# Optimization experiments

Hardware: AMD Instinct MI355X
Metric: run time of the kernel (lower is better)

Reference implementation:

```python
import jax, jax.numpy as jnp
import numpy as np

N, S, E, H = 2, 2048, 1024, 16
D = E // H  # head_dim = 64


def setup_inputs() -> dict:
    key = jax.random.key(0)
    k1, k2, k3 = jax.random.split(key, 3)
    x = jax.random.normal(k1, (N, S, E), dtype=jnp.float32)
    # Xavier-uniform-scaled weights (torch Linear layout: [out_features, in_features])
    lim_qkv = (6.0 / (E + 3 * E)) ** 0.5
    qkv_w = jax.random.uniform(k2, (3 * E, E), dtype=jnp.float32, minval=-lim_qkv, maxval=lim_qkv)
    lim_o = (6.0 / (E + E)) ** 0.5
    o_w = jax.random.uniform(k3, (E, E), dtype=jnp.float32, minval=-lim_o, maxval=lim_o)
    # causal look-ahead mask: positions where mask == 0 are excluded
    attn_mask = jnp.tril(jnp.ones((S, S), dtype=jnp.int32))
    return {"x": x, "attn_mask": attn_mask, "qkv_w": qkv_w, "o_w": o_w}


def reference(x, attn_mask, qkv_w, o_w):
    n, s, e = x.shape
    qkv = x @ qkv_w.T                              # (N, S, 3E)
    q, k, v = jnp.split(qkv, 3, axis=-1)
    # (N, S, E) -> (N, H, S, D)
    def to_heads(t):
        return t.reshape(n, s, H, D).transpose(0, 2, 1, 3)
    q, k, v = to_heads(q), to_heads(k), to_heads(v)
    scale = 1.0 / jnp.sqrt(jnp.asarray(D, dtype=x.dtype))
    logits = jnp.einsum('bhqd,bhkd->bhqk', q, k) * scale   # (N, H, S, S)
    mask = attn_mask.reshape(1, 1, s, s)                    # expand_mask: 2D -> (1,1,S,S)
    logits = jnp.where(mask == 0, -jnp.inf, logits)
    attn_weights = jax.nn.softmax(logits, axis=-1)
    values = jnp.einsum('bhqk,bhkd->bhqd', attn_weights, v)  # (N, H, S, D)
    values = values.transpose(0, 2, 1, 3).reshape(n, s, e)
    o = values @ o_w.T
    return o
```

## Files before the change

### kernel.cpp

```cpp
#include <hip/hip_runtime.h>
#include <math.h>

typedef unsigned short u16;
typedef unsigned int uint;
typedef __attribute__((ext_vector_type(8))) short bf16x8;
typedef __attribute__((ext_vector_type(8))) _Float16 half8;
typedef __attribute__((ext_vector_type(2))) _Float16 half2t;
typedef __attribute__((ext_vector_type(4))) float floatx4;

__device__ __forceinline__ u16 f2bf(float f) {
  union { float f; uint u; } c; c.f = f;
  return (u16)((c.u + 0x7FFFu + ((c.u >> 16) & 1u)) >> 16);
}
__device__ __forceinline__ float bf2f(u16 h) {
  union { uint u; float f; } c; c.u = ((uint)h) << 16;
  return c.f;
}
__device__ __forceinline__ u16 h2u(_Float16 h) {
  union { _Float16 h; u16 u; } c; c.h = h;
  return c.u;
}

#if __has_builtin(__builtin_amdgcn_exp2f)
#define EX2 __builtin_amdgcn_exp2f
#else
#define EX2 exp2f
#endif

__device__ __forceinline__ void gl_lds16(const u16* g, u16* l) {
  __builtin_amdgcn_global_load_lds(
      (const __attribute__((address_space(1))) uint*)g,
      (__attribute__((address_space(3))) uint*)l, 16, 0, 0);
}

__device__ __forceinline__ void store_c(u16* p, float v) { *p = f2bf(v); }
__device__ __forceinline__ void store_c(float* p, float v) { *p = v; }

#define ROR16(x, n)                                                        \
  __builtin_bit_cast(float, __builtin_amdgcn_update_dpp(                   \
      __builtin_bit_cast(int, (x)), __builtin_bit_cast(int, (x)),          \
      0x120 + (n), 0xF, 0xF, false))
__device__ __forceinline__ float rsum16(float x) {
  x += ROR16(x, 8); x += ROR16(x, 4); x += ROR16(x, 2); x += ROR16(x, 1);
  return x;
}

__global__ __launch_bounds__(256) void cvt_all(const float* __restrict__ x,
                                               const float* __restrict__ qw,
                                               const float* __restrict__ ow,
                                               u16* __restrict__ xb,
                                               u16* __restrict__ wb,
                                               u16* __restrict__ ob) {
  int bx = blockIdx.x;
  const float* src; u16* dst; int off;
  if (bx < 2048) { src = x; dst = xb; off = bx; }
  else if (bx < 3584) { src = qw; dst = wb; off = bx - 2048; }
  else { src = ow; dst = ob; off = bx - 3584; }
  int i = (off * 256 + threadIdx.x) * 8;
  float4 a = *(const float4*)(src + i);
  float4 b = *(const float4*)(src + i + 4);
  bf16x8 r;
  r[0] = (short)f2bf(a.x); r[1] = (short)f2bf(a.y);
  r[2] = (short)f2bf(a.z); r[3] = (short)f2bf(a.w);
  r[4] = (short)f2bf(b.x); r[5] = (short)f2bf(b.y);
  r[6] = (short)f2bf(b.z); r[7] = (short)f2bf(b.w);
  *(bf16x8*)(dst + i) = r;
}

__global__ __launch_bounds__(256) void vtrans(const u16* __restrict__ qkv,
                                              u16* __restrict__ vt) {
  constexpr int S = 2048, E = 1024, TE = 3072;
  __shared__ u16 tile[64 * 72];
  const int t = threadIdx.x;
  const int kv0 = blockIdx.x * 64;
  const int bh = blockIdx.y, b = bh >> 4, h = bh & 15;
  const u16* src = qkv + (size_t)b * S * TE + 2 * E + h * 64;
#pragma unroll
  for (int i = 0; i < 2; ++i) {
    int c = t + i * 256;
    int kv = c >> 3, d0 = (c & 7) * 8;
    *(bf16x8*)&tile[kv * 72 + d0] = *(const bf16x8*)&src[(size_t)(kv0 + kv) * TE + d0];
  }
  __syncthreads();
  u16* dst = vt + (size_t)bh * 64 * S + kv0;
#pragma unroll
  for (int i = 0; i < 2; ++i) {
    int c = t + i * 256;
    int d = c >> 3, k0 = (c & 7) * 8;
    bf16x8 r;
#pragma unroll
    for (int j = 0; j < 8; ++j)
      r[j] = (short)h2u((_Float16)bf2f(tile[(k0 + j) * 72 + d]));
    *(bf16x8*)&dst[(size_t)d * S + k0] = r;
  }
}

template <typename TC>
__global__ __launch_bounds__(256) void gemm_bt(const u16* __restrict__ A,
                                               const u16* __restrict__ B,
                                               TC* __restrict__ C,
                                               int K, int N) {
  __shared__ __align__(16) u16 lds_a[128 * 64];
  __shared__ __align__(16) u16 lds_b[128 * 64];
  const int t = threadIdx.x;
  const int w = t >> 6, lane = t & 63, quad = lane >> 4, lr = lane & 15;
  const int wr = w >> 1, wc = w & 1;
  const int m0 = blockIdx.y * 128, n0 = blockIdx.x * 128;

  const int srow = lane >> 3;
  const int scol = ((lane & 7) ^ srow) * 8;
  const u16* Ab = A + (size_t)(m0 + w * 32 + srow) * K + scol;
  const u16* Bb = B + (size_t)(n0 + w * 32 + srow) * K + scol;
  u16* la = lds_a + (w * 32) * 64;
  u16* lb = lds_b + (w * 32) * 64;

  floatx4 acc[4][4];
#pragma unroll
  for (int i = 0; i < 4; ++i)
#pragma unroll
    for (int j = 0; j < 4; ++j) acc[i][j] = {0.f, 0.f, 0.f, 0.f};

  for (int k0 = 0; k0 < K; k0 += 64) {
#pragma unroll
    for (int j = 0; j < 4; ++j) {
      gl_lds16(Ab + (size_t)(j * 8) * K + k0, la + j * 8 * 64);
      gl_lds16(Bb + (size_t)(j * 8) * K + k0, lb + j * 8 * 64);
    }
    __syncthreads();
#pragma unroll
    for (int kk = 0; kk < 2; ++kk) {
      bf16x8 af[4], bfr[4];
#pragma unroll
      for (int mi = 0; mi < 4; ++mi)
        af[mi] = *(const bf16x8*)&lds_a[(wr * 64 + mi * 16 + lr) * 64 +
                                        (((kk * 4 + quad) ^ (lr & 7)) * 8)];
#pragma unroll
      for (int ni = 0; ni < 4; ++ni)
        bfr[ni] = *(const bf16x8*)&lds_b[(wc * 64 + ni * 16 + lr) * 64 +
                                         (((kk * 4 + quad) ^ (lr & 7)) * 8)];
#pragma unroll
      for (int mi = 0; mi < 4; ++mi)
#pragma unroll
        for (int ni = 0; ni < 4; ++ni)
          acc[mi][ni] = __builtin_amdgcn_mfma_f32_16x16x32_bf16(
              af[mi], bfr[ni], acc[mi][ni], 0, 0, 0);
    }
    __syncthreads();
  }
#pragma unroll
  for (int mi = 0; mi < 4; ++mi)
#pragma unroll
    for (int r = 0; r < 4; ++r) {
      int m = m0 + wr * 64 + mi * 16 + quad * 4 + r;
#pragma unroll
      for (int ni = 0; ni < 4; ++ni) {
        int n = n0 + wc * 64 + ni * 16 + lr;
        store_c(&C[(size_t)m * N + n], acc[mi][ni][r]);
      }
    }
}

template <typename TC>
__global__ __launch_bounds__(256) void gemm_bt64(const u16* __restrict__ A,
                                                 const u16* __restrict__ B,
                                                 TC* __restrict__ C,
                                                 int K, int N) {
  __shared__ __align__(16) u16 lds_a[64 * 64];
  __shared__ __align__(16) u16 lds_b[128 * 64];
  const int t = threadIdx.x;
  const int w = t >> 6, lane = t & 63, quad = lane >> 4, lr = lane & 15;
  const int m0 = blockIdx.y * 64, n0 = blockIdx.x * 128;

  const int srow = lane >> 3;
  const int scol = ((lane & 7) ^ srow) * 8;
  const u16* Ab = A + (size_t)(m0 + srow) * K + scol;
  const u16* Bb = B + (size_t)(n0 + srow) * K + scol;

  floatx4 acc[4][2];
#pragma unroll
  for (int i = 0; i < 4; ++i)
#pragma unroll
    for (int j = 0; j < 2; ++j) acc[i][j] = {0.f, 0.f, 0.f, 0.f};

  for (int k0 = 0; k0 < K; k0 += 64) {
#pragma unroll
    for (int i = 0; i < 2; ++i)
      gl_lds16(Ab + (size_t)((w * 2 + i) * 8) * K + k0, &lds_a[(w * 2 + i) * 8 * 64]);
#pragma unroll
    for (int i = 0; i < 4; ++i)
      gl_lds16(Bb + (size_t)((w * 4 + i) * 8) * K + k0, &lds_b[(w * 4 + i) * 8 * 64]);
    __syncthreads();
#pragma unroll
    for (int kk = 0; kk < 2; ++kk) {
      bf16x8 af[4], bfr[2];
#pragma unroll
      for (int mi = 0; mi < 4; ++mi)
        af[mi] = *(const bf16x8*)&lds_a[(mi * 16 + lr) * 64 +
                                        (((kk * 4 + quad) ^ (lr & 7)) * 8)];
#pragma unroll
      for (int ni = 0; ni < 2; ++ni)
        bfr[ni] = *(const bf16x8*)&lds_b[(w * 32 + ni * 16 + lr) * 64 +
                                         (((kk * 4 + quad) ^ (lr & 7)) * 8)];
#pragma unroll
      for (int mi = 0; mi < 4; ++mi)
#pragma unroll
        for (int ni = 0; ni < 2; ++ni)
          acc[mi][ni] = __builtin_amdgcn_mfma_f32_16x16x32_bf16(
              af[mi], bfr[ni], acc[mi][ni], 0, 0, 0);
    }
    __syncthreads();
  }
#pragma unroll
  for (int mi = 0; mi < 4; ++mi)
#pragma unroll
    for (int r = 0; r < 4; ++r) {
      int m = m0 + mi * 16 + quad * 4 + r;
#pragma unroll
      for (int ni = 0; ni < 2; ++ni) {
        int n = n0 + w * 32 + ni * 16 + lr;
        store_c(&C[(size_t)m * N + n], acc[mi][ni][r]);
      }
    }
}

__global__ __launch_bounds__(256, 2) void attn_fwd(const u16* __restrict__ qkv,
                                                   const u16* __restrict__ vt,
                                                   u16* __restrict__ out,
                                                   float* __restrict__ opart,
                                                   float* __restrict__ lpart) {
  constexpr int S = 2048, E = 1024, TE = 3072;
  constexpr float NEG = -1e30f;
  __shared__ __align__(16) u16 lds_k[2][128 * 64];
  __shared__ __align__(16) u16 lds_vt[2][64 * 128];
  const int t = threadIdx.x;
  const int w = t >> 6, lane = t & 63, quad = lane >> 4, lr = lane & 15;
  const int bx = (int)blockIdx.x;
  const int h = bx & 15, pr = (bx >> 4) & 7, hB = (bx >> 7) & 1, b = bx >> 8;
  const int qtH = 15 - pr;
  const int bh = b * 16 + h;
  const int pid = bh * 8 + pr;
  const size_t base = (size_t)b * S * TE;
  const u16* kbase = qkv + base + E + h * 64;
  const u16* vtb = vt + (size_t)bh * 64 * S;

  const int s8 = lane >> 3;
  const int kcol = ((lane & 7) ^ s8) * 8;
  const int vrow = lane >> 4;

  const int n0 = hB ? (8 - pr) : 8;
  const int niter = hB ? 9 : 8;

  const float QS = 0.125f * 1.44269504f;
  bf16x8 qf[2][2];
  float lst2[2];
  floatx4 oacc[2][4];

  auto load_q = [&](int qt) {
#pragma unroll
    for (int rg = 0; rg < 2; ++rg)
#pragma unroll
      for (int kk = 0; kk < 2; ++kk) {
        bf16x8 q = *(const bf16x8*)&qkv[base +
            (size_t)(qt * 128 + w * 32 + rg * 16 + lr) * TE + h * 64 + kk * 32 + quad * 8];
#pragma unroll
        for (int jj = 0; jj < 8; ++jj) q[jj] = (short)f2bf(bf2f((u16)q[jj]) * QS);
        qf[rg][kk] = q;
      }
  };
  auto reset_acc = [&]() {
    lst2[0] = 0.f; lst2[1] = 0.f;
#pragma unroll
    for (int rg = 0; rg < 2; ++rg)
#pragma unroll
      for (int di = 0; di < 4; ++di) oacc[rg][di] = {0.f, 0.f, 0.f, 0.f};
  };
  auto reduce_l = [&](float* lred) {
#pragma unroll
    for (int rg = 0; rg < 2; ++rg) {
      float x = lst2[rg];
      x += __shfl_xor(x, 16);
      x += __shfl_xor(x, 32);
      lred[rg] = x;
    }
  };
  auto emit_partial = [&](int slot) {
    float lred[2];
    reduce_l(lred);
    float* op = opart + ((size_t)slot * 256 + pid) * (128 * 64);
    float* lp = lpart + ((size_t)slot * 256 + pid) * 128;
    if (quad == 0) lp[w * 32 + lr] = lred[0];
    if (quad == 1) lp[w * 32 + 16 + lr] = lred[1];
#pragma unroll
    for (int rg = 0; rg < 2; ++rg)
#pragma unroll
      for (int r = 0; r < 4; ++r) {
        int row = w * 32 + rg * 16 + quad * 4 + r;
#pragma unroll
        for (int di = 0; di < 4; ++di)
          op[row * 64 + di * 16 + lr] = oacc[rg][di][r];
      }
  };
  auto kv_of = [&](int it) -> int {
    if (!hB) return it;
    return (it < n0) ? (8 + it) : (it - n0);
  };
  auto stage = [&](int kvt, int bi) {
    int nb = kvt * 128;
#pragma unroll
    for (int i = 0; i < 4; ++i) {
      int p0 = w * 8 + i * 32;
      int p = p0 + s8;
      int kv = ((p >> 5) & 3) * 32 + ((p >> 2) & 3) * 8 + ((p >> 4) & 1) * 4 + (p & 3);
      gl_lds16(kbase + (size_t)(nb + kv) * TE + kcol, &lds_k[bi][p0 * 64]);
    }
#pragma unroll
    for (int i = 0; i < 4; ++i) {
      int d0 = w * 4 + i * 16;
      int d = d0 + vrow;
      int cbg = ((lane & 15) ^ (d & 15)) * 8;
      gl_lds16(vtb + (size_t)d * S + nb + cbg, &lds_vt[bi][d0 * 128]);
    }
  };

  load_q(qtH);
  stage(kv_of(0), 0);
  reset_acc();

  for (int it = 0; it < niter; ++it) {
    const int cur = it & 1;
    const int kt = kv_of(it);
    const int qcur = (hB && it >= n0) ? pr : qtH;

    asm volatile("s_waitcnt vmcnt(0)\n\ts_barrier" ::: "memory");
    __builtin_amdgcn_sched_barrier(0);

    floatx4 st[2][8];
#pragma unroll
    for (int rg = 0; rg < 2; ++rg)
#pragma unroll
      for (int ni = 0; ni < 8; ++ni) st[rg][ni] = {-4.f, -4.f, -4.f, -4.f};
    __builtin_amdgcn_s_setprio(1);
#pragma unroll
    for (int kk = 0; kk < 2; ++kk) {
      bf16x8 kb[8];
#pragma unroll
      for (int ni = 0; ni < 8; ++ni)
        kb[ni] = *(const bf16x8*)&lds_k[cur][(ni * 16 + lr) * 64 +
                                            (((kk * 4 + quad) ^ (lr & 7)) * 8)];
#pragma unroll
      for (int rg = 0; rg < 2; ++rg)
#pragma unroll
        for (int ni = 0; ni < 8; ++ni)
          st[rg][ni] = __builtin_amdgcn_mfma_f32_16x16x32_bf16(
              kb[ni], qf[rg][kk], st[rg][ni], 0, 0, 0);
    }
    __builtin_amdgcn_s_setprio(0);

    half8 vb[4][4];
#pragma unroll
    for (int kk = 0; kk < 4; ++kk)
#pragma unroll
      for (int di = 0; di < 4; ++di)
        vb[kk][di] = *(const half8*)&lds_vt[cur][(di * 16 + lr) * 128 +
                                                 (((kk * 4 + quad) ^ lr) << 3)];

    if (it + 1 < niter) stage(kv_of(it + 1), cur ^ 1);

    const bool diag = (kt == qcur);
#pragma unroll
    for (int rg = 0; rg < 2; ++rg) {
      const int rloc = w * 32 + rg * 16 + lr;
      float ex[8][4];
#pragma unroll
      for (int ni = 0; ni < 8; ++ni)
#pragma unroll
        for (int rr = 0; rr < 4; ++rr) {
          float s = st[rg][ni][rr];
          if (diag) {
            int kvl = ((ni >> 1) << 5) + (quad << 3) + ((ni & 1) << 2) + rr;
            if (kvl > rloc) s = NEG;
          }
          ex[ni][rr] = EX2(s);
        }
      float tsum[8];
#pragma unroll
      for (int ni = 0; ni < 8; ++ni)
        tsum[ni] = (ex[ni][0] + ex[ni][1]) + (ex[ni][2] + ex[ni][3]);
      lst2[rg] += ((tsum[0] + tsum[1]) + (tsum[2] + tsum[3])) +
                  ((tsum[4] + tsum[5]) + (tsum[6] + tsum[7]));
      __builtin_amdgcn_s_setprio(1);
#pragma unroll
      for (int c = 0; c < 4; ++c) {
        union { half2t h2[4]; half8 h8; } pu;
        pu.h2[0] = __builtin_bit_cast(half2t,
            __builtin_amdgcn_cvt_pkrtz(ex[2 * c][0], ex[2 * c][1]));
        pu.h2[1] = __builtin_bit_cast(half2t,
            __builtin_amdgcn_cvt_pkrtz(ex[2 * c][2], ex[2 * c][3]));
        pu.h2[2] = __builtin_bit_cast(half2t,
            __builtin_amdgcn_cvt_pkrtz(ex[2 * c + 1][0], ex[2 * c + 1][1]));
        pu.h2[3] = __builtin_bit_cast(half2t,
            __builtin_amdgcn_cvt_pkrtz(ex[2 * c + 1][2], ex[2 * c + 1][3]));
#pragma unroll
        for (int di = 0; di < 4; ++di)
          oacc[rg][di] = __builtin_amdgcn_mfma_f32_16x16x32_f16(
              pu.h8, vb[c][di], oacc[rg][di], 0, 0, 0);
      }
      __builtin_amdgcn_s_setprio(0);
    }

    if (hB && it == n0 - 1) {
      emit_partial(1);
      reset_acc();
      load_q(pr);
    }
  }

  if (!hB) {
    emit_partial(0);
  } else {
    float lred[2];
    reduce_l(lred);
#pragma unroll
    for (int rg = 0; rg < 2; ++rg)
#pragma unroll
      for (int r = 0; r < 4; ++r) {
        int sg = pr * 128 + w * 32 + rg * 16 + quad * 4 + r;
        float lrow = __shfl(lred[rg], quad * 4 + r);
        float inv_l = 1.f / lrow;
#pragma unroll
        for (int di = 0; di < 4; ++di)
          out[((size_t)(b * S + sg)) * E + h * 64 + di * 16 + lr] =
              f2bf(oacc[rg][di][r] * inv_l);
      }
  }
}

__global__ __launch_bounds__(256) void attn_combine(const float* __restrict__ opart,
                                                    const float* __restrict__ lpart,
                                                    u16* __restrict__ out) {
  constexpr int S = 2048, E = 1024;
  const int p = (int)blockIdx.x;
  const int pr = p & 7, bh = p >> 3, h = bh & 15, b = bh >> 4;
  const int q0 = (15 - pr) * 128;
  const int t = threadIdx.x;
  const int row = t >> 1, c0 = (t & 1) * 32;
  const float* o0 = opart + (size_t)p * (128 * 64) + row * 64 + c0;
  const float* o1 = o0 + (size_t)256 * 128 * 64;
  float l = lpart[p * 128 + row] + lpart[256 * 128 + p * 128 + row];
  float inv = 1.f / l;
  u16* dst = out + ((size_t)(b * S + q0 + row)) * E + h * 64 + c0;
#pragma unroll
  for (int i = 0; i < 4; ++i) {
    float4 a0 = ((const float4*)o0)[2 * i], a1 = ((const float4*)o0)[2 * i + 1];
    float4 b0 = ((const float4*)o1)[2 * i], b1 = ((const float4*)o1)[2 * i + 1];
    bf16x8 r;
    r[0] = (short)f2bf((a0.x + b0.x) * inv);
    r[1] = (short)f2bf((a0.y + b0.y) * inv);
    r[2] = (short)f2bf((a0.z + b0.z) * inv);
    r[3] = (short)f2bf((a0.w + b0.w) * inv);
    r[4] = (short)f2bf((a1.x + b1.x) * inv);
    r[5] = (short)f2bf((a1.y + b1.y) * inv);
    r[6] = (short)f2bf((a1.z + b1.z) * inv);
    r[7] = (short)f2bf((a1.w + b1.w) * inv);
    ((bf16x8*)dst)[i] = r;
  }
}

extern "C" void kernel_launch(void* const* d_in, const int* in_sizes, int n_in,
                              void* d_out, int out_size, void* d_ws, size_t ws_size,
                              hipStream_t stream) {
  constexpr int NB = 2, S = 2048, E = 1024;
  constexpr int M = NB * S;
  const float* x = (const float*)d_in[0];
  const float* qkv_w = (const float*)d_in[2];
  const float* o_w = (const float*)d_in[3];
  float* out = (float*)d_out;

  u16* qkv = (u16*)d_ws;
  u16* vt = qkv + (size_t)M * 3 * E;
  u16* xb = vt + (size_t)32 * 64 * S;
  u16* attn_o = xb;
  u16* wb = xb + (size_t)M * E;
  u16* ob = wb + (size_t)3 * E * E;
  float* opart = (float*)(ob + (size_t)E * E);
  float* lpart = opart + (size_t)2 * 256 * 128 * 64;

  cvt_all<<<4096, 256, 0, stream>>>(x, qkv_w, o_w, xb, wb, ob);
  gemm_bt<u16><<<dim3(3 * E / 128, M / 128), 256, 0, stream>>>(xb, wb, qkv, E, 3 * E);
  vtrans<<<dim3(S / 64, NB * 16), 256, 0, stream>>>(qkv, vt);
  attn_fwd<<<512, 256, 0, stream>>>(qkv, vt, attn_o, opart, lpart);
  attn_combine<<<256, 256, 0, stream>>>(opart, lpart, attn_o);
  gemm_bt64<float><<<dim3(E / 128, M / 64), 256, 0, stream>>>(attn_o, ob, out, E, E);
}
```

Measured before the change: 198.6 us.

## Split causal attention into four KV chunks per pair with atomic accumulation

The attention work for each pair of query tiles (17 KV tiles) is now split across four blocks instead of two, giving 1024 blocks. Each block adds its unnormalized output and row sums into a zeroed global fp32 buffer with atomicAdd, and a normalize kernel writes the bf16 result. LDS is single-buffered with an extra barrier, and launch bounds ask for four blocks per CU, which trades load/compute overlap for occupancy. The change adds a memset, atomic traffic and non-deterministic summation order.

New measurement: 502.8 us. 2.53x slower.

```diff
diff --git a/kernel.cpp b/kernel.cpp
--- a/kernel.cpp
+++ b/kernel.cpp
@@ -35,15 +35,6 @@
 
 __device__ __forceinline__ void store_c(u16* p, float v) { *p = f2bf(v); }
 __device__ __forceinline__ void store_c(float* p, float v) { *p = v; }
-
-#define ROR16(x, n)                                                        \
-  __builtin_bit_cast(float, __builtin_amdgcn_update_dpp(                   \
-      __builtin_bit_cast(int, (x)), __builtin_bit_cast(int, (x)),          \
-      0x120 + (n), 0xF, 0xF, false))
-__device__ __forceinline__ float rsum16(float x) {
-  x += ROR16(x, 8); x += ROR16(x, 4); x += ROR16(x, 2); x += ROR16(x, 1);
-  return x;
-}
 
 __global__ __launch_bounds__(256) void cvt_all(const float* __restrict__ x,
                                                const float* __restrict__ qw,
@@ -223,22 +214,20 @@
     }
 }
 
-__global__ __launch_bounds__(256, 2) void attn_fwd(const u16* __restrict__ qkv,
+__global__ __launch_bounds__(256, 4) void attn_fwd(const u16* __restrict__ qkv,
                                                    const u16* __restrict__ vt,
-                                                   u16* __restrict__ out,
-                                                   float* __restrict__ opart,
-                                                   float* __restrict__ lpart) {
+                                                   float* __restrict__ oaccg,
+                                                   float* __restrict__ laccg) {
   constexpr int S = 2048, E = 1024, TE = 3072;
   constexpr float NEG = -1e30f;
-  __shared__ __align__(16) u16 lds_k[2][128 * 64];
-  __shared__ __align__(16) u16 lds_vt[2][64 * 128];
+  __shared__ __align__(16) u16 lds_k[128 * 64];
+  __shared__ __align__(16) u16 lds_vt[64 * 128];
   const int t = threadIdx.x;
   const int w = t >> 6, lane = t & 63, quad = lane >> 4, lr = lane & 15;
   const int bx = (int)blockIdx.x;
-  const int h = bx & 15, pr = (bx >> 4) & 7, hB = (bx >> 7) & 1, b = bx >> 8;
+  const int h = bx & 15, qr = (bx >> 4) & 3, pr = (bx >> 6) & 7, b = bx >> 9;
   const int qtH = 15 - pr;
   const int bh = b * 16 + h;
-  const int pid = bh * 8 + pr;
   const size_t base = (size_t)b * S * TE;
   const u16* kbase = qkv + base + E + h * 64;
   const u16* vtb = vt + (size_t)bh * 64 * S;
@@ -247,8 +236,9 @@
   const int kcol = ((lane & 7) ^ s8) * 8;
   const int vrow = lane >> 4;
 
-  const int n0 = hB ? (8 - pr) : 8;
-  const int niter = hB ? 9 : 8;
+  const int fs = qr * 4;
+  const int fe = (qr == 3) ? 17 : fs + 4;
+  const int bnd = 16 - pr;
 
   const float QS = 0.125f * 1.44269504f;
   bf16x8 qf[2][2];
@@ -283,13 +273,13 @@
       lred[rg] = x;
     }
   };
-  auto emit_partial = [&](int slot) {
+  auto emit_atomic = [&](int qt) {
     float lred[2];
     reduce_l(lred);
-    float* op = opart + ((size_t)slot * 256 + pid) * (128 * 64);
-    float* lp = lpart + ((size_t)slot * 256 + pid) * 128;
-    if (quad == 0) lp[w * 32 + lr] = lred[0];
-    if (quad == 1) lp[w * 32 + 16 + lr] = lred[1];
+    float* oa = oaccg + ((size_t)(bh * 16 + qt)) * (128 * 64);
+    float* la = laccg + (bh * 16 + qt) * 128;
+    if (quad == 0) atomicAdd(&la[w * 32 + lr], lred[0]);
+    if (quad == 1) atomicAdd(&la[w * 32 + 16 + lr], lred[1]);
 #pragma unroll
     for (int rg = 0; rg < 2; ++rg)
 #pragma unroll
@@ -297,40 +287,33 @@
         int row = w * 32 + rg * 16 + quad * 4 + r;
 #pragma unroll
         for (int di = 0; di < 4; ++di)
-          op[row * 64 + di * 16 + lr] = oacc[rg][di][r];
+          atomicAdd(&oa[row * 64 + di * 16 + lr], oacc[rg][di][r]);
       }
   };
-  auto kv_of = [&](int it) -> int {
-    if (!hB) return it;
-    return (it < n0) ? (8 + it) : (it - n0);
-  };
-  auto stage = [&](int kvt, int bi) {
+  auto stage = [&](int kvt) {
     int nb = kvt * 128;
 #pragma unroll
     for (int i = 0; i < 4; ++i) {
       int p0 = w * 8 + i * 32;
       int p = p0 + s8;
       int kv = ((p >> 5) & 3) * 32 + ((p >> 2) & 3) * 8 + ((p >> 4) & 1) * 4 + (p & 3);
-      gl_lds16(kbase + (size_t)(nb + kv) * TE + kcol, &lds_k[bi][p0 * 64]);
+      gl_lds16(kbase + (size_t)(nb + kv) * TE + kcol, &lds_k[p0 * 64]);
     }
 #pragma unroll
     for (int i = 0; i < 4; ++i) {
       int d0 = w * 4 + i * 16;
       int d = d0 + vrow;
       int cbg = ((lane & 15) ^ (d & 15)) * 8;
-      gl_lds16(vtb + (size_t)d * S + nb + cbg, &lds_vt[bi][d0 * 128]);
+      gl_lds16(vtb + (size_t)d * S + nb + cbg, &lds_vt[d0 * 128]);
     }
   };
 
-  load_q(qtH);
-  stage(kv_of(0), 0);
+  int qcur = (fs < bnd) ? qtH : pr;
+  load_q(qcur);
   reset_acc();
-
-  for (int it = 0; it < niter; ++it) {
-    const int cur = it & 1;
-    const int kt = kv_of(it);
-    const int qcur = (hB && it >= n0) ? pr : qtH;
-
+  stage((fs < bnd) ? fs : fs - bnd);
+
+  for (int f = fs; f < fe; ++f) {
     asm volatile("s_waitcnt vmcnt(0)\n\ts_barrier" ::: "memory");
     __builtin_amdgcn_sched_barrier(0);
 
@@ -345,8 +328,8 @@
       bf16x8 kb[8];
 #pragma unroll
       for (int ni = 0; ni < 8; ++ni)
-        kb[ni] = *(const bf16x8*)&lds_k[cur][(ni * 16 + lr) * 64 +
-                                            (((kk * 4 + quad) ^ (lr & 7)) * 8)];
+        kb[ni] = *(const bf16x8*)&lds_k[(ni * 16 + lr) * 64 +
+                                        (((kk * 4 + quad) ^ (lr & 7)) * 8)];
 #pragma unroll
       for (int rg = 0; rg < 2; ++rg)
 #pragma unroll
@@ -361,12 +344,18 @@
     for (int kk = 0; kk < 4; ++kk)
 #pragma unroll
       for (int di = 0; di < 4; ++di)
-        vb[kk][di] = *(const half8*)&lds_vt[cur][(di * 16 + lr) * 128 +
-                                                 (((kk * 4 + quad) ^ lr) << 3)];
-
-    if (it + 1 < niter) stage(kv_of(it + 1), cur ^ 1);
-
-    const bool diag = (kt == qcur);
+        vb[kk][di] = *(const half8*)&lds_vt[(di * 16 + lr) * 128 +
+                                            (((kk * 4 + quad) ^ lr) << 3)];
+
+    asm volatile("s_waitcnt lgkmcnt(0)\n\ts_barrier" ::: "memory");
+    __builtin_amdgcn_sched_barrier(0);
+
+    if (f + 1 < fe) {
+      int f2 = f + 1;
+      stage((f2 < bnd) ? f2 : f2 - bnd);
+    }
+
+    const bool diag = (f == bnd - 1) || (f == 16);
 #pragma unroll
     for (int rg = 0; rg < 2; ++rg) {
       const int rloc = w * 32 + rg * 16 + lr;
@@ -408,60 +397,40 @@
       __builtin_amdgcn_s_setprio(0);
     }
 
-    if (hB && it == n0 - 1) {
-      emit_partial(1);
+    if (f == bnd - 1 && f + 1 < fe) {
+      emit_atomic(qtH);
       reset_acc();
       load_q(pr);
-    }
-  }
-
-  if (!hB) {
-    emit_partial(0);
-  } else {
-    float lred[2];
-    reduce_l(lred);
-#pragma unroll
-    for (int rg = 0; rg < 2; ++rg)
-#pragma unroll
-      for (int r = 0; r < 4; ++r) {
-        int sg = pr * 128 + w * 32 + rg * 16 + quad * 4 + r;
-        float lrow = __shfl(lred[rg], quad * 4 + r);
-        float inv_l = 1.f / lrow;
-#pragma unroll
-        for (int di = 0; di < 4; ++di)
-          out[((size_t)(b * S + sg)) * E + h * 64 + di * 16 + lr] =
-              f2bf(oacc[rg][di][r] * inv_l);
-      }
-  }
-}
-
-__global__ __launch_bounds__(256) void attn_combine(const float* __restrict__ opart,
-                                                    const float* __restrict__ lpart,
-                                                    u16* __restrict__ out) {
+      qcur = pr;
+    }
+  }
+
+  emit_atomic(qcur);
+}
+
+__global__ __launch_bounds__(256) void attn_norm(const float* __restrict__ oaccg,
+                                                 const float* __restrict__ laccg,
+                                                 u16* __restrict__ out) {
   constexpr int S = 2048, E = 1024;
   const int p = (int)blockIdx.x;
-  const int pr = p & 7, bh = p >> 3, h = bh & 15, b = bh >> 4;
-  const int q0 = (15 - pr) * 128;
+  const int qt = p & 15, bh = p >> 4, h = bh & 15, b = bh >> 4;
   const int t = threadIdx.x;
   const int row = t >> 1, c0 = (t & 1) * 32;
-  const float* o0 = opart + (size_t)p * (128 * 64) + row * 64 + c0;
-  const float* o1 = o0 + (size_t)256 * 128 * 64;
-  float l = lpart[p * 128 + row] + lpart[256 * 128 + p * 128 + row];
-  float inv = 1.f / l;
-  u16* dst = out + ((size_t)(b * S + q0 + row)) * E + h * 64 + c0;
+  const float* o = oaccg + (size_t)p * (128 * 64) + row * 64 + c0;
+  float inv = 1.f / laccg[p * 128 + row];
+  u16* dst = out + ((size_t)(b * S + qt * 128 + row)) * E + h * 64 + c0;
 #pragma unroll
   for (int i = 0; i < 4; ++i) {
-    float4 a0 = ((const float4*)o0)[2 * i], a1 = ((const float4*)o0)[2 * i + 1];
-    float4 b0 = ((const float4*)o1)[2 * i], b1 = ((const float4*)o1)[2 * i + 1];
+    float4 a0 = ((const float4*)o)[2 * i], a1 = ((const float4*)o)[2 * i + 1];
     bf16x8 r;
-    r[0] = (short)f2bf((a0.x + b0.x) * inv);
-    r[1] = (short)f2bf((a0.y + b0.y) * inv);
-    r[2] = (short)f2bf((a0.z + b0.z) * inv);
-    r[3] = (short)f2bf((a0.w + b0.w) * inv);
-    r[4] = (short)f2bf((a1.x + b1.x) * inv);
-    r[5] = (short)f2bf((a1.y + b1.y) * inv);
-    r[6] = (short)f2bf((a1.z + b1.z) * inv);
-    r[7] = (short)f2bf((a1.w + b1.w) * inv);
+    r[0] = (short)f2bf(a0.x * inv);
+    r[1] = (short)f2bf(a0.y * inv);
+    r[2] = (short)f2bf(a0.z * inv);
+    r[3] = (short)f2bf(a0.w * inv);
+    r[4] = (short)f2bf(a1.x * inv);
+    r[5] = (short)f2bf(a1.y * inv);
+    r[6] = (short)f2bf(a1.z * inv);
+    r[7] = (short)f2bf(a1.w * inv);
     ((bf16x8*)dst)[i] = r;
   }
 }
@@ -482,13 +451,16 @@
   u16* attn_o = xb;
   u16* wb = xb + (size_t)M * E;
   u16* ob = wb + (size_t)3 * E * E;
-  float* opart = (float*)(ob + (size_t)E * E);
-  float* lpart = opart + (size_t)2 * 256 * 128 * 64;
-
+  float* oaccg = (float*)(ob + (size_t)E * E);
+  float* laccg = oaccg + (size_t)32 * 16 * 128 * 64;
+
+  hipMemsetAsync(oaccg, 0,
+                 ((size_t)32 * 16 * 128 * 64 + (size_t)32 * 16 * 128) * 4,
+                 stream);
   cvt_all<<<4096, 256, 0, stream>>>(x, qkv_w, o_w, xb, wb, ob);
   gemm_bt<u16><<<dim3(3 * E / 128, M / 128), 256, 0, stream>>>(xb, wb, qkv, E, 3 * E);
   vtrans<<<dim3(S / 64, NB * 16), 256, 0, stream>>>(qkv, vt);
-  attn_fwd<<<512, 256, 0, stream>>>(qkv, vt, attn_o, opart, lpart);
-  attn_combine<<<256, 256, 0, stream>>>(opart, lpart, attn_o);
+  attn_fwd<<<1024, 256, 0, stream>>>(qkv, vt, oaccg, laccg);
+  attn_norm<<<512, 256, 0, stream>>>(oaccg, laccg, attn_o);
   gemm_bt64<float><<<dim3(E / 128, M / 64), 256, 0, stream>>>(attn_o, ob, out, E, E);
 }
```
